# Kernel optimization log

Hardware: AMD Instinct MI355X
Metric: run time of the kernel (lower is better)

Reference implementation:

```python
import jax, jax.numpy as jnp
import numpy as np

N = 100000      # nodes
E = 1600000     # edges (no self-loops by construction)
DIN, DH, DOUT = 128, 128, 64
EPS = 1e-8      # torch cosine_similarity eps
LN_EPS = 1e-5


def _segsum(v, idx, n=N):
    return jax.ops.segment_sum(v, idx, num_segments=n)


def att_coef(feats, row, col):
    """Edge-wise cosine-sim attention + degree norm + self-loop append (torch no_grad block).
    Returns fixed-shape (row2, col2, vals2) of length E+N; filtered edges get weight 0
    (equivalent to removal for all scatter_add / message-passing math)."""
    dot = jnp.einsum('ed,ed->e', feats[row], feats[col])            # [E]
    nrm = jnp.maximum(jnp.linalg.norm(feats, axis=1), EPS)          # [N]
    sims = dot / (nrm[row] * nrm[col])
    keep = sims >= 0.1                                              # row!=col guaranteed
    sims = jnp.where(keep, sims, 0.0)
    deg = _segsum(sims, row)
    dinv = jnp.where(deg > 0, deg ** -0.5, 0.0)                     # inf -> 0
    sims = dinv[row] * sims * dinv[col]
    deg_new = _segsum(keep.astype(feats.dtype), col) + 1.0          # [N], >= 1
    self_val = 1.0 / deg_new
    vals = jnp.where(keep, jnp.exp(sims), 0.0)                      # removed edges -> 0
    sl = jnp.arange(N)
    row2 = jnp.concatenate([row, sl])
    col2 = jnp.concatenate([col, sl])
    vals2 = jnp.concatenate([vals, jnp.exp(self_val)])
    return row2, col2, vals2


def gcn_conv(x, row, col, w, W, b):
    """PyG GCNConv (normalize=True, add_self_loops=False) with given edge_weight."""
    h = x @ W                                                        # [N, out]
    deg = _segsum(w, col)
    dinv = jnp.where(deg > 0, deg ** -0.5, 0.0)
    norm = dinv[row] * w * dinv[col]                                 # [E+N]
    out = _segsum(norm[:, None] * h[row], col)                       # scatter to targets
    return out + b


def layer_norm(x, g, b):
    mu = jnp.mean(x, axis=-1, keepdims=True)
    var = jnp.mean((x - mu) ** 2, axis=-1, keepdims=True)
    return (x - mu) * jax.lax.rsqrt(var + LN_EPS) * g + b


def setup_inputs() -> dict:
    key = jax.random.key(0)
    ks = jax.random.split(key, 6)
    x = jax.random.normal(ks[0], (N, DIN), jnp.float32)
    row = jax.random.randint(ks[1], (E,), 0, N)
    col = jax.random.randint(ks[2], (E,), 0, N)
    col = jnp.where(col == row, (col + 1) % N, col)                  # no self-loops
    s1 = float(np.sqrt(6.0 / (DIN + DH)))                            # glorot
    s2 = float(np.sqrt(6.0 / (DH + DOUT)))
    W1 = jax.random.uniform(ks[3], (DIN, DH), jnp.float32, -s1, s1)
    W2 = jax.random.uniform(ks[4], (DH, DOUT), jnp.float32, -s2, s2)
    return dict(x=x, row=row, col=col,
                W1=W1, b1=jnp.zeros((DH,), jnp.float32),
                ln_g=jnp.ones((DH,), jnp.float32), ln_b=jnp.zeros((DH,), jnp.float32),
                W2=W2, b2=jnp.zeros((DOUT,), jnp.float32))


def reference(x, row, col, W1, b1, ln_g, ln_b, W2, b2):
    # layer 1: att_coef (no_grad) -> GCNConv -> LayerNorm -> ReLU (dropout is eval no-op)
    r2, c2, v2 = att_coef(jax.lax.stop_gradient(x), row, col)
    h = gcn_conv(x, r2, c2, v2, W1, b1)
    h = jax.nn.relu(layer_norm(h, ln_g, ln_b))
    # layer 2: att_coef on updated features (original edge list), final conv + log_softmax
    r2, c2, v2 = att_coef(jax.lax.stop_gradient(h), row, col)
    out = gcn_conv(h, r2, c2, v2, W2, b2)
    return jax.nn.log_softmax(out, axis=-1)
```

## Files before the change

### kernel.cpp

```cpp
#include <hip/hip_runtime.h>
#include <math.h>

#define EPSF 1e-8f
#define LN_EPS 1e-5f
#define BL_MARGIN 0.002f

#define BKT_SH 9
#define CHUNK 4096
#define DCAP 16384

typedef unsigned int  u32;
typedef unsigned short u16;
typedef _Float16 h2_t __attribute__((ext_vector_type(2)));
typedef _Float16 half8_t __attribute__((ext_vector_type(8)));
typedef float f32x4_t __attribute__((ext_vector_type(4)));

static __device__ inline u32 pack_h2(float a, float b) {
    h2_t h; h.x = (_Float16)a; h.y = (_Float16)b;
    return __builtin_bit_cast(u32, h);
}
static __device__ inline float h2lo(u32 u) {
    return (float)__builtin_bit_cast(h2_t, u).x;
}
static __device__ inline float h2hi(u32 u) {
    return (float)__builtin_bit_cast(h2_t, u).y;
}

static __device__ inline f32x4_t mfma16(uint4 a, uint4 b, f32x4_t c) {
    return __builtin_amdgcn_mfma_f32_16x16x32_f16(
        __builtin_bit_cast(half8_t, a), __builtin_bit_cast(half8_t, b), c, 0, 0, 0);
}

__global__ __launch_bounds__(256) void cast_norm_k(const float* __restrict__ feat,
    u32* __restrict__ fhf, float* __restrict__ nrm, int n) {
    int wid  = (blockIdx.x * 256 + threadIdx.x) >> 6;
    int lane = threadIdx.x & 63;
    if (wid >= n) return;
    float2 v = *(const float2*)(feat + (size_t)wid * 128 + lane * 2);
    float s = v.x * v.x + v.y * v.y;
    #pragma unroll
    for (int off = 32; off; off >>= 1) s += __shfl_xor(s, off, 64);
    float nv = fmaxf(sqrtf(s), EPSF);
    float inv = 1.0f / nv;
    fhf[(size_t)wid * 64 + lane] = pack_h2(v.x * inv, v.y * inv);
    if (lane == 0) nrm[wid] = nv;
}


__global__ __launch_bounds__(256) void hist_k(const int* __restrict__ col,
                                              int* __restrict__ bcnt, int ecnt) {
    __shared__ int lc[256];
    lc[threadIdx.x] = 0; __syncthreads();
    for (int e = blockIdx.x * 256 + threadIdx.x; e < ecnt; e += gridDim.x * 256)
        atomicAdd(&lc[col[e] >> BKT_SH], 1);
    __syncthreads();
    int v = lc[threadIdx.x];
    if (v) atomicAdd(&bcnt[threadIdx.x], v);
}

__global__ __launch_bounds__(256) void bscan_k(const int* __restrict__ bcnt,
    int* __restrict__ bstart, int* __restrict__ bcur) {
    __shared__ int tmp[256];
    int t = threadIdx.x;
    int v = bcnt[t];
    tmp[t] = v; __syncthreads();
    for (int off = 1; off < 256; off <<= 1) {
        int a = (t >= off) ? tmp[t - off] : 0;
        __syncthreads();
        tmp[t] += a;
        __syncthreads();
    }
    int ex = tmp[t] - v;
    bstart[t] = ex; bcur[t] = ex;
    if (t == 255) bstart[256] = tmp[255];
}

__global__ __launch_bounds__(256) void binfill_k(const int* __restrict__ row,
    const int* __restrict__ col, int* __restrict__ bcur,
    int2* __restrict__ ebuf, int ecnt) {
    __shared__ int lc[256], ls[256], cur[256], gbase[256];
    __shared__ int2 pairs[CHUNK];
    __shared__ int dstv[CHUNK];
    int t = threadIdx.x;
    int e0 = blockIdx.x * CHUNK;
    int m = min(CHUNK, ecnt - e0);
    lc[t] = 0; cur[t] = 0; __syncthreads();
    int myc[CHUNK / 256], myr[CHUNK / 256];
    #pragma unroll
    for (int i = 0; i < CHUNK / 256; ++i) {
        int idx = t + i * 256;
        if (idx < m) {
            myc[i] = col[e0 + idx];
            myr[i] = row[e0 + idx];
            atomicAdd(&lc[myc[i] >> BKT_SH], 1);
        }
    }
    __syncthreads();
    int v = lc[t];
    ls[t] = v; __syncthreads();
    for (int off = 1; off < 256; off <<= 1) {
        int a = (t >= off) ? ls[t - off] : 0;
        __syncthreads();
        ls[t] += a;
        __syncthreads();
    }
    int ex = ls[t] - v;
    __syncthreads();
    ls[t] = ex;
    if (v) gbase[t] = atomicAdd(&bcur[t], v);
    __syncthreads();
    #pragma unroll
    for (int i = 0; i < CHUNK / 256; ++i) {
        int idx = t + i * 256;
        if (idx < m) {
            int b = myc[i] >> BKT_SH;
            int s = ls[b] + atomicAdd(&cur[b], 1);
            pairs[s] = make_int2(myc[i], myr[i]);
            dstv[s]  = gbase[b] + (s - ls[b]);
        }
    }
    __syncthreads();
    for (int s = t; s < m; s += 256)
        ebuf[dstv[s]] = pairs[s];
}

__global__ __launch_bounds__(256) void bucket_csr_k(const int2* __restrict__ ebuf,
    const int* __restrict__ bstart, int* __restrict__ startAll,
    int* __restrict__ cntAll, int* __restrict__ rowAll, int n) {
    __shared__ int cnt[512], lst[512], cur[512];
    __shared__ int rowbuf[DCAP];
    int b = blockIdx.x, t = threadIdx.x;
    int c0 = b << BKT_SH;
    int s0 = bstart[b], s1 = bstart[b + 1];
    int m = s1 - s0;
    cnt[t] = 0; cnt[t + 256] = 0; cur[t] = 0; cur[t + 256] = 0;
    __syncthreads();
    for (int i = t; i < m; i += 256)
        atomicAdd(&cnt[ebuf[s0 + i].x - c0], 1);
    __syncthreads();
    int v0 = cnt[t], v1 = cnt[t + 256];
    lst[t] = v0; lst[t + 256] = v1; __syncthreads();
    for (int off = 1; off < 256; off <<= 1) {
        int a0 = (t >= off) ? lst[t - off] : 0;
        int a1 = (t >= off) ? lst[256 + t - off] : 0;
        __syncthreads();
        lst[t] += a0; lst[t + 256] += a1;
        __syncthreads();
    }
    int h0 = lst[255];
    int e0x = lst[t] - v0;
    int e1x = lst[t + 256] - v1 + h0;
    __syncthreads();
    lst[t] = e0x; lst[t + 256] = e1x;
    __syncthreads();
    #pragma unroll
    for (int half = 0; half < 2; ++half) {
        int i = t + half * 256;
        int c = c0 + i;
        if (c < n) { startAll[c] = s0 + lst[i]; cntAll[c] = cnt[i]; }
    }
    if (m <= DCAP) {
        for (int i = t; i < m; i += 256) {
            int2 p = ebuf[s0 + i];
            int ci = p.x - c0;
            int pos = lst[ci] + atomicAdd(&cur[ci], 1);
            rowbuf[pos] = p.y;
        }
        __syncthreads();
        for (int i = t; i < m; i += 256)
            rowAll[s0 + i] = rowbuf[i];
    } else {
        for (int i = t; i < m; i += 256) {
            int2 p = ebuf[s0 + i];
            int ci = p.x - c0;
            int pos = lst[ci] + atomicAdd(&cur[ci], 1);
            rowAll[s0 + pos] = p.y;
        }
    }
}

__global__ __launch_bounds__(256) void edge_dot_mf_k(const u32* __restrict__ fhf,
    const float* __restrict__ feat32,
    const int* __restrict__ rowAll, const int* __restrict__ startAll,
    const int* __restrict__ cntAll, const float* __restrict__ nrm,
    float* __restrict__ sims, float* __restrict__ deg1, int n) {
    int wid  = (blockIdx.x * 256 + threadIdx.x) >> 6;
    int lane = threadIdx.x & 63;
    if (wid >= n) return;
    int s0 = startAll[wid], cnt = cntAll[wid];
    if (cnt == 0) return;
    int lr = lane & 15;
    int kq = lane >> 4;
    const u32* fcp = fhf + (size_t)wid * 64 + kq * 4;
    uint4 a0 = *(const uint4*)(fcp);
    uint4 a1 = *(const uint4*)(fcp + 16);
    uint4 a2 = *(const uint4*)(fcp + 32);
    uint4 a3 = *(const uint4*)(fcp + 48);
    float nc = nrm[wid];
    int cm1 = cnt - 1;
    for (int jj = 0; jj < cnt; jj += 32) {
        int e1 = jj + lr;
        int r1 = rowAll[s0 + min(e1, cm1)];
        const u32* fr1 = fhf + (size_t)r1 * 64 + kq * 4;
        uint4 b0 = *(const uint4*)(fr1);
        uint4 b1 = *(const uint4*)(fr1 + 16);
        uint4 b2 = *(const uint4*)(fr1 + 32);
        uint4 b3 = *(const uint4*)(fr1 + 48);
        bool g2 = (jj + 16) < cnt;
        int e2 = jj + 16 + lr;
        int r2 = 0;
        uint4 c0, c1, c2, c3;
        if (g2) {
            r2 = rowAll[s0 + min(e2, cm1)];
            const u32* fr2 = fhf + (size_t)r2 * 64 + kq * 4;
            c0 = *(const uint4*)(fr2);
            c1 = *(const uint4*)(fr2 + 16);
            c2 = *(const uint4*)(fr2 + 32);
            c3 = *(const uint4*)(fr2 + 48);
        }
        f32x4_t acc = {0.f, 0.f, 0.f, 0.f};
        acc = mfma16(a0, b0, acc);
        acc = mfma16(a1, b1, acc);
        acc = mfma16(a2, b2, acc);
        acc = mfma16(a3, b3, acc);
        float p1 = acc[0];
        bool act1 = (kq == 0) && (e1 < cnt);
        float p2 = 0.0f;
        bool act2 = false;
        if (g2) {
            f32x4_t acc2 = {0.f, 0.f, 0.f, 0.f};
            acc2 = mfma16(a0, c0, acc2);
            acc2 = mfma16(a1, c1, acc2);
            acc2 = mfma16(a2, c2, acc2);
            acc2 = mfma16(a3, c3, acc2);
            p2 = acc2[0];
            act2 = (kq == 0) && (e2 < cnt);
        }
        unsigned long long bl = __ballot(act1 && fabsf(p1 - 0.1f) < BL_MARGIN);
        while (bl) {
            int src = __ffsll((unsigned long long)bl) - 1; bl &= bl - 1ull;
            int rt = __shfl(r1, src, 64);
            float2 xa = *(const float2*)(feat32 + (size_t)rt * 128 + lane * 2);
            float2 xb = *(const float2*)(feat32 + (size_t)wid * 128 + lane * 2);
            float s2 = xa.x * xb.x + xa.y * xb.y;
            #pragma unroll
            for (int off = 32; off; off >>= 1) s2 += __shfl_xor(s2, off, 64);
            float pf = s2 / (nrm[rt] * nc);
            if (lane == src) p1 = pf;
        }
        unsigned long long bl2 = __ballot(act2 && fabsf(p2 - 0.1f) < BL_MARGIN);
        while (bl2) {
            int src = __ffsll((unsigned long long)bl2) - 1; bl2 &= bl2 - 1ull;
            int rt = __shfl(r2, src, 64);
            float2 xa = *(const float2*)(feat32 + (size_t)rt * 128 + lane * 2);
            float2 xb = *(const float2*)(feat32 + (size_t)wid * 128 + lane * 2);
            float s2 = xa.x * xb.x + xa.y * xb.y;
            #pragma unroll
            for (int off = 32; off; off >>= 1) s2 += __shfl_xor(s2, off, 64);
            float pf = s2 / (nrm[rt] * nc);
            if (lane == src) p2 = pf;
        }
        if (act1) {
            float kv = (p1 >= 0.1f) ? p1 : 0.0f;
            sims[s0 + e1] = kv;
            if (kv > 0.0f) atomicAdd(&deg1[r1], kv);
        }
        if (act2) {
            float kv = (p2 >= 0.1f) ? p2 : 0.0f;
            sims[s0 + e2] = kv;
            if (kv > 0.0f) atomicAdd(&deg1[r2], kv);
        }
    }
}

__global__ __launch_bounds__(256) void edge_c_csr_k(const float* __restrict__ sims,
    const int* __restrict__ rowAll, const int* __restrict__ startAll,
    const int* __restrict__ cntAll, const float* __restrict__ deg1,
    int2* __restrict__ kv, int* __restrict__ cntK, float* __restrict__ dinv2,
    float* __restrict__ cself, int n) {
    int wid  = (blockIdx.x * 256 + threadIdx.x) >> 6;
    int lane = threadIdx.x & 63;
    if (wid >= n) return;
    int s0 = startAll[wid], cnt = cntAll[wid];
    float degc = deg1[wid];
    float d1c = (degc > 0.0f) ? 1.0f / sqrtf(degc) : 0.0f;
    float vsum = 0.0f; int kc = 0;
    for (int jj = 0; jj < cnt; jj += 64) {
        int j = jj + lane;
        bool keep = false; int r = 0; float v = 0.0f;
        if (j < cnt) {
            float s = sims[s0 + j];
            if (s > 0.0f) {
                r = rowAll[s0 + j];
                float dr = 1.0f / sqrtf(deg1[r]);
                v = expf(dr * s * d1c);
                keep = true;
            }
        }
        unsigned long long m = __ballot(keep ? 1 : 0);
        if (keep) {
            int pre = __popcll(m & ((1ull << lane) - 1ull));
            int2 pk; pk.x = r; pk.y = __float_as_int(v);
            kv[s0 + kc + pre] = pk;
            vsum += v;
        }
        kc += __popcll(m);
    }
    #pragma unroll
    for (int off = 32; off; off >>= 1) vsum += __shfl_xor(vsum, off, 64);
    if (lane == 0) {
        float ws_ = expf(1.0f / ((float)kc + 1.0f));
        float dg = ws_ + vsum;
        float di = 1.0f / sqrtf(dg);
        dinv2[wid] = di;
        cself[wid] = di * ws_;
        cntK[wid]  = kc;
    }
}


__global__ __launch_bounds__(256) void gemm128_k(const float* __restrict__ A,
    const float* __restrict__ W, const float* __restrict__ scale,
    float* __restrict__ out, int n) {
    __shared__ float Ws[128 * 64];
    int colBase = blockIdx.y * 64;
    for (int i = threadIdx.x; i < 128 * 64 / 4; i += 256) {
        int k = i >> 4, c4 = i & 15;
        ((float4*)Ws)[i] = *(const float4*)(W + k * 128 + colBase + c4 * 4);
    }
    __syncthreads();
    const int TPN = 16;
    int group = threadIdx.x / TPN;
    int tin   = threadIdx.x % TPN;
    int nid   = (blockIdx.x * 16 + group) * 4;
    if (nid >= n) return;
    int dbase = tin * 4;
    int nm1 = n - 1;
    const float4* a0 = (const float4*)(A + (size_t)min(nid,     nm1) * 128);
    const float4* a1 = (const float4*)(A + (size_t)min(nid + 1, nm1) * 128);
    const float4* a2 = (const float4*)(A + (size_t)min(nid + 2, nm1) * 128);
    const float4* a3 = (const float4*)(A + (size_t)min(nid + 3, nm1) * 128);
    float4 acc0 = {0,0,0,0}, acc1 = {0,0,0,0}, acc2 = {0,0,0,0}, acc3 = {0,0,0,0};
    #pragma unroll 2
    for (int k4 = 0; k4 < 32; ++k4) {
        const float* wr = Ws + (k4 * 4) * 64 + dbase;
        float4 w0 = *(const float4*)(wr);
        float4 w1 = *(const float4*)(wr + 64);
        float4 w2 = *(const float4*)(wr + 128);
        float4 w3 = *(const float4*)(wr + 192);
        float4 v0 = a0[k4], v1 = a1[k4], v2 = a2[k4], v3 = a3[k4];
        acc0.x += v0.x*w0.x + v0.y*w1.x + v0.z*w2.x + v0.w*w3.x;
        acc0.y += v0.x*w0.y + v0.y*w1.y + v0.z*w2.y + v0.w*w3.y;
        acc0.z += v0.x*w0.z + v0.y*w1.z + v0.z*w2.z + v0.w*w3.z;
        acc0.w += v0.x*w0.w + v0.y*w1.w + v0.z*w2.w + v0.w*w3.w;
        acc1.x += v1.x*w0.x + v1.y*w1.x + v1.z*w2.x + v1.w*w3.x;
        acc1.y += v1.x*w0.y + v1.y*w1.y + v1.z*w2.y + v1.w*w3.y;
        acc1.z += v1.x*w0.z + v1.y*w1.z + v1.z*w2.z + v1.w*w3.z;
        acc1.w += v1.x*w0.w + v1.y*w1.w + v1.z*w2.w + v1.w*w3.w;
        acc2.x += v2.x*w0.x + v2.y*w1.x + v2.z*w2.x + v2.w*w3.x;
        acc2.y += v2.x*w0.y + v2.y*w1.y + v2.z*w2.y + v2.w*w3.y;
        acc2.z += v2.x*w0.z + v2.y*w1.z + v2.z*w2.z + v2.w*w3.z;
        acc2.w += v2.x*w0.w + v2.y*w1.w + v2.z*w2.w + v2.w*w3.w;
        acc3.x += v3.x*w0.x + v3.y*w1.x + v3.z*w2.x + v3.w*w3.x;
        acc3.y += v3.x*w0.y + v3.y*w1.y + v3.z*w2.y + v3.w*w3.y;
        acc3.z += v3.x*w0.z + v3.y*w1.z + v3.z*w2.z + v3.w*w3.z;
        acc3.w += v3.x*w0.w + v3.y*w1.w + v3.z*w2.w + v3.w*w3.w;
    }
    float4 accs[4] = {acc0, acc1, acc2, acc3};
    #pragma unroll
    for (int i = 0; i < 4; ++i) {
        if (nid + i < n) {
            float sc = scale[nid + i];
            float4 r; r.x = accs[i].x * sc; r.y = accs[i].y * sc;
            r.z = accs[i].z * sc; r.w = accs[i].w * sc;
            *(float4*)(out + (size_t)(nid + i) * 128 + colBase + dbase) = r;
        }
    }
}

__global__ __launch_bounds__(256) void gemm64_hf_k(const float* __restrict__ A,
    const float* __restrict__ W, const float* __restrict__ scale,
    u32* __restrict__ outhf, int n) {
    __shared__ float Ws[128 * 32];
    int colBase = blockIdx.y * 32;
    for (int i = threadIdx.x; i < 128 * 32 / 4; i += 256) {
        int k = i >> 3, c4 = i & 7;
        ((float4*)Ws)[i] = *(const float4*)(W + k * 64 + colBase + c4 * 4);
    }
    __syncthreads();
    const int TPN = 8;
    int group = threadIdx.x / TPN;
    int tin   = threadIdx.x % TPN;
    int nid   = (blockIdx.x * 32 + group) * 4;
    if (nid >= n) return;
    int dbase = tin * 4;
    int nm1 = n - 1;
    const float4* a0 = (const float4*)(A + (size_t)min(nid,     nm1) * 128);
    const float4* a1 = (const float4*)(A + (size_t)min(nid + 1, nm1) * 128);
    const float4* a2 = (const float4*)(A + (size_t)min(nid + 2, nm1) * 128);
    const float4* a3 = (const float4*)(A + (size_t)min(nid + 3, nm1) * 128);
    float4 acc0 = {0,0,0,0}, acc1 = {0,0,0,0}, acc2 = {0,0,0,0}, acc3 = {0,0,0,0};
    #pragma unroll 2
    for (int k4 = 0; k4 < 32; ++k4) {
        const float* wr = Ws + (k4 * 4) * 32 + dbase;
        float4 w0 = *(const float4*)(wr);
        float4 w1 = *(const float4*)(wr + 32);
        float4 w2 = *(const float4*)(wr + 64);
        float4 w3 = *(const float4*)(wr + 96);
        float4 v0 = a0[k4], v1 = a1[k4], v2 = a2[k4], v3 = a3[k4];
        acc0.x += v0.x*w0.x + v0.y*w1.x + v0.z*w2.x + v0.w*w3.x;
        acc0.y += v0.x*w0.y + v0.y*w1.y + v0.z*w2.y + v0.w*w3.y;
        acc0.z += v0.x*w0.z + v0.y*w1.z + v0.z*w2.z + v0.w*w3.z;
        acc0.w += v0.x*w0.w + v0.y*w1.w + v0.z*w2.w + v0.w*w3.w;
        acc1.x += v1.x*w0.x + v1.y*w1.x + v1.z*w2.x + v1.w*w3.x;
        acc1.y += v1.x*w0.y + v1.y*w1.y + v1.z*w2.y + v1.w*w3.y;
        acc1.z += v1.x*w0.z + v1.y*w1.z + v1.z*w2.z + v1.w*w3.z;
        acc1.w += v1.x*w0.w + v1.y*w1.w + v1.z*w2.w + v1.w*w3.w;
        acc2.x += v2.x*w0.x + v2.y*w1.x + v2.z*w2.x + v2.w*w3.x;
        acc2.y += v2.x*w0.y + v2.y*w1.y + v2.z*w2.y + v2.w*w3.y;
        acc2.z += v2.x*w0.z + v2.y*w1.z + v2.z*w2.z + v2.w*w3.z;
        acc2.w += v2.x*w0.w + v2.y*w1.w + v2.z*w2.w + v2.w*w3.w;
        acc3.x += v3.x*w0.x + v3.y*w1.x + v3.z*w2.x + v3.w*w3.x;
        acc3.y += v3.x*w0.y + v3.y*w1.y + v3.z*w2.y + v3.w*w3.y;
        acc3.z += v3.x*w0.z + v3.y*w1.z + v3.z*w2.z + v3.w*w3.z;
        acc3.w += v3.x*w0.w + v3.y*w1.w + v3.z*w2.w + v3.w*w3.w;
    }
    float4 accs[4] = {acc0, acc1, acc2, acc3};
    #pragma unroll
    for (int i = 0; i < 4; ++i) {
        if (nid + i < n) {
            float sc = scale[nid + i];
            u32 o0 = pack_h2(accs[i].x * sc, accs[i].y * sc);
            u32 o1 = pack_h2(accs[i].z * sc, accs[i].w * sc);
            *(uint2*)(outhf + (size_t)(nid + i) * 32 + (colBase >> 1) + tin * 2)
                = make_uint2(o0, o1);
        }
    }
}


__global__ __launch_bounds__(256) void gather_ln_k(const float* __restrict__ hs,
    const int2* __restrict__ kv, const int* __restrict__ startAll,
    const int* __restrict__ cntK, const float* __restrict__ dinv2,
    const float* __restrict__ cself, const float* __restrict__ bias,
    const float* __restrict__ g, const float* __restrict__ bln,
    float* __restrict__ outbuf, u32* __restrict__ outhf,
    float* __restrict__ nrm, int n) {
    int wid = (blockIdx.x * 256 + threadIdx.x) >> 5;
    int l   = threadIdx.x & 31;
    if (wid >= n) return;
    int s0 = startAll[wid], k = cntK[wid];
    float4 acc = {0,0,0,0};
    int j = 0;
    for (; j + 7 < k; j += 8) {
        int2 p0 = kv[s0+j],   p1 = kv[s0+j+1], p2 = kv[s0+j+2], p3 = kv[s0+j+3];
        int2 p4 = kv[s0+j+4], p5 = kv[s0+j+5], p6 = kv[s0+j+6], p7 = kv[s0+j+7];
        float4 h0 = *(const float4*)(hs + (size_t)p0.x * 128 + l * 4);
        float4 h1 = *(const float4*)(hs + (size_t)p1.x * 128 + l * 4);
        float4 h2v = *(const float4*)(hs + (size_t)p2.x * 128 + l * 4);
        float4 h3 = *(const float4*)(hs + (size_t)p3.x * 128 + l * 4);
        float4 h4 = *(const float4*)(hs + (size_t)p4.x * 128 + l * 4);
        float4 h5 = *(const float4*)(hs + (size_t)p5.x * 128 + l * 4);
        float4 h6 = *(const float4*)(hs + (size_t)p6.x * 128 + l * 4);
        float4 h7 = *(const float4*)(hs + (size_t)p7.x * 128 + l * 4);
        float v0 = __int_as_float(p0.y), v1 = __int_as_float(p1.y);
        float v2 = __int_as_float(p2.y), v3 = __int_as_float(p3.y);
        float v4 = __int_as_float(p4.y), v5 = __int_as_float(p5.y);
        float v6 = __int_as_float(p6.y), v7 = __int_as_float(p7.y);
        acc.x += v0*h0.x + v1*h1.x + v2*h2v.x + v3*h3.x
               + v4*h4.x + v5*h5.x + v6*h6.x + v7*h7.x;
        acc.y += v0*h0.y + v1*h1.y + v2*h2v.y + v3*h3.y
               + v4*h4.y + v5*h5.y + v6*h6.y + v7*h7.y;
        acc.z += v0*h0.z + v1*h1.z + v2*h2v.z + v3*h3.z
               + v4*h4.z + v5*h5.z + v6*h6.z + v7*h7.z;
        acc.w += v0*h0.w + v1*h1.w + v2*h2v.w + v3*h3.w
               + v4*h4.w + v5*h5.w + v6*h6.w + v7*h7.w;
    }
    for (; j < k; ++j) {
        int2 p0 = kv[s0 + j];
        float4 h0 = *(const float4*)(hs + (size_t)p0.x * 128 + l * 4);
        float v0 = __int_as_float(p0.y);
        acc.x += v0*h0.x; acc.y += v0*h0.y; acc.z += v0*h0.z; acc.w += v0*h0.w;
    }
    float di = dinv2[wid], cs = cself[wid];
    float4 hsv = *(const float4*)(hs + (size_t)wid * 128 + l * 4);
    float4 vb  = *(const float4*)(bias + l * 4);
    float x0 = di*acc.x + cs*hsv.x + vb.x;
    float x1 = di*acc.y + cs*hsv.y + vb.y;
    float x2 = di*acc.z + cs*hsv.z + vb.z;
    float x3 = di*acc.w + cs*hsv.w + vb.w;
    float s = x0 + x1 + x2 + x3;
    #pragma unroll
    for (int off = 16; off; off >>= 1) s += __shfl_xor(s, off, 64);
    float mu = s * (1.0f / 128.0f);
    float d0 = x0 - mu, d1 = x1 - mu, d2 = x2 - mu, d3 = x3 - mu;
    float vv = d0*d0 + d1*d1 + d2*d2 + d3*d3;
    #pragma unroll
    for (int off = 16; off; off >>= 1) vv += __shfl_xor(vv, off, 64);
    float rstd = 1.0f / sqrtf(vv * (1.0f / 128.0f) + LN_EPS);
    float4 vg  = *(const float4*)(g + l * 4);
    float4 vbl = *(const float4*)(bln + l * 4);
    float y0 = fmaxf(d0 * rstd * vg.x + vbl.x, 0.0f);
    float y1 = fmaxf(d1 * rstd * vg.y + vbl.y, 0.0f);
    float y2 = fmaxf(d2 * rstd * vg.z + vbl.z, 0.0f);
    float y3 = fmaxf(d3 * rstd * vg.w + vbl.w, 0.0f);
    float4 yo; yo.x = y0; yo.y = y1; yo.z = y2; yo.w = y3;
    *(float4*)(outbuf + (size_t)wid * 128 + l * 4) = yo;
    float ns = y0*y0 + y1*y1 + y2*y2 + y3*y3;
    #pragma unroll
    for (int off = 16; off; off >>= 1) ns += __shfl_xor(ns, off, 64);
    float nv = fmaxf(sqrtf(ns), EPSF);
    float inv = 1.0f / nv;
    uint2 oh; oh.x = pack_h2(y0 * inv, y1 * inv); oh.y = pack_h2(y2 * inv, y3 * inv);
    *(uint2*)(outhf + (size_t)wid * 64 + l * 2) = oh;
    if (l == 0) nrm[wid] = nv;
}

__global__ __launch_bounds__(256) void gather_lsm_hf_k(const u32* __restrict__ g2s,
    const int2* __restrict__ kv, const int* __restrict__ startAll,
    const int* __restrict__ cntK, const float* __restrict__ dinv2,
    const float* __restrict__ cself, const float* __restrict__ b2,
    float* __restrict__ out, int n) {
    int wid = (blockIdx.x * 256 + threadIdx.x) >> 5;
    int l   = threadIdx.x & 31;
    if (wid >= n) return;
    int s0 = startAll[wid], k = cntK[wid];
    float acc0 = 0.f, acc1 = 0.f;
    int j = 0;
    for (; j + 7 < k; j += 8) {
        int2 p0 = kv[s0+j],   p1 = kv[s0+j+1], p2 = kv[s0+j+2], p3 = kv[s0+j+3];
        int2 p4 = kv[s0+j+4], p5 = kv[s0+j+5], p6 = kv[s0+j+6], p7 = kv[s0+j+7];
        u32 g0 = g2s[(size_t)p0.x * 32 + l];
        u32 g1 = g2s[(size_t)p1.x * 32 + l];
        u32 g2 = g2s[(size_t)p2.x * 32 + l];
        u32 g3 = g2s[(size_t)p3.x * 32 + l];
        u32 g4 = g2s[(size_t)p4.x * 32 + l];
        u32 g5 = g2s[(size_t)p5.x * 32 + l];
        u32 g6 = g2s[(size_t)p6.x * 32 + l];
        u32 g7 = g2s[(size_t)p7.x * 32 + l];
        float v0 = __int_as_float(p0.y), v1 = __int_as_float(p1.y);
        float v2 = __int_as_float(p2.y), v3 = __int_as_float(p3.y);
        float v4 = __int_as_float(p4.y), v5 = __int_as_float(p5.y);
        float v6 = __int_as_float(p6.y), v7 = __int_as_float(p7.y);
        acc0 += v0*h2lo(g0) + v1*h2lo(g1) + v2*h2lo(g2) + v3*h2lo(g3)
              + v4*h2lo(g4) + v5*h2lo(g5) + v6*h2lo(g6) + v7*h2lo(g7);
        acc1 += v0*h2hi(g0) + v1*h2hi(g1) + v2*h2hi(g2) + v3*h2hi(g3)
              + v4*h2hi(g4) + v5*h2hi(g5) + v6*h2hi(g6) + v7*h2hi(g7);
    }
    for (; j < k; ++j) {
        int2 p0 = kv[s0 + j];
        u32 g0 = g2s[(size_t)p0.x * 32 + l];
        float v0 = __int_as_float(p0.y);
        acc0 += v0 * h2lo(g0); acc1 += v0 * h2hi(g0);
    }
    float di = dinv2[wid], cs = cself[wid];
    u32 gsu = g2s[(size_t)wid * 32 + l];
    float2 vb = *(const float2*)(b2 + l * 2);
    float v0 = di * acc0 + cs * h2lo(gsu) + vb.x;
    float v1 = di * acc1 + cs * h2hi(gsu) + vb.y;
    float m = fmaxf(v0, v1);
    #pragma unroll
    for (int off = 16; off; off >>= 1) m = fmaxf(m, __shfl_xor(m, off, 64));
    float e = expf(v0 - m) + expf(v1 - m);
    #pragma unroll
    for (int off = 16; off; off >>= 1) e += __shfl_xor(e, off, 64);
    float lse = m + logf(e);
    *(float2*)(out + (size_t)wid * 64 + l * 2) = make_float2(v0 - lse, v1 - lse);
}


extern "C" void kernel_launch(void* const* d_in, const int* in_sizes, int n_in,
                              void* d_out, int out_size, void* d_ws, size_t ws_size,
                              hipStream_t stream) {
    (void)n_in; (void)out_size; (void)ws_size;
    const float* x   = (const float*)d_in[0];
    const int*   row = (const int*)d_in[1];
    const int*   col = (const int*)d_in[2];
    const float* W1  = (const float*)d_in[3];
    const float* b1  = (const float*)d_in[4];
    const float* lng = (const float*)d_in[5];
    const float* lnb = (const float*)d_in[6];
    const float* W2  = (const float*)d_in[7];
    const float* b2  = (const float*)d_in[8];
    float* out = (float*)d_out;

    const int N = in_sizes[0] / 128;
    const int E = in_sizes[1];

    int*   cntAll   = (int*)d_ws;
    int*   startAll = cntAll + N;
    int*   bcnt     = startAll + N;
    int*   bstart   = bcnt + 256;
    int*   bcur     = bstart + 257;
    float* nrm      = (float*)(bcnt + 1024);
    float* deg1     = nrm + N;
    float* dinv2    = deg1 + N;
    float* cself    = dinv2 + N;
    int*   cntK     = (int*)(cself + N);
    int*   rowAll   = cntK + N;
    int2*  kvp      = (int2*)(rowAll + E);
    u32*   fhf      = (u32*)(kvp + E);
    u32*   g2shf    = fhf + (size_t)64 * N;
    float* big      = (float*)(g2shf + (size_t)32 * N);
    float* sims     = big;
    float* hs       = big;
    float* h2       = big + (size_t)128 * N;
    int2*  ebuf     = kvp;

    const int waveBlocks  = (N + 3) / 4;
    const int halfBlocks  = (N + 7) / 8;
    const int NB          = (N + 511) >> 9;

    hipMemsetAsync(bcnt, 0, 256 * sizeof(int), stream);
    hist_k<<<256, 256, 0, stream>>>(col, bcnt, E);
    bscan_k<<<1, 256, 0, stream>>>(bcnt, bstart, bcur);
    binfill_k<<<(E + CHUNK - 1) / CHUNK, 256, 0, stream>>>(row, col, bcur, ebuf, E);
    bucket_csr_k<<<NB, 256, 0, stream>>>(ebuf, bstart, startAll, cntAll, rowAll, N);

    hipMemsetAsync(deg1, 0, (size_t)N * sizeof(float), stream);
    cast_norm_k<<<waveBlocks, 256, 0, stream>>>(x, fhf, nrm, N);
    edge_dot_mf_k<<<waveBlocks, 256, 0, stream>>>(fhf, x, rowAll, startAll, cntAll, nrm,
                                                  sims, deg1, N);
    edge_c_csr_k<<<waveBlocks, 256, 0, stream>>>(sims, rowAll, startAll, cntAll, deg1,
                                                 kvp, cntK, dinv2, cself, N);
    gemm128_k<<<dim3((N + 63) / 64, 2), 256, 0, stream>>>(x, W1, dinv2, hs, N);
    gather_ln_k<<<halfBlocks, 256, 0, stream>>>(hs, kvp, startAll, cntK, dinv2, cself,
                                                b1, lng, lnb, h2, fhf, nrm, N);

    hipMemsetAsync(deg1, 0, (size_t)N * sizeof(float), stream);
    edge_dot_mf_k<<<waveBlocks, 256, 0, stream>>>(fhf, h2, rowAll, startAll, cntAll, nrm,
                                                  sims, deg1, N);
    edge_c_csr_k<<<waveBlocks, 256, 0, stream>>>(sims, rowAll, startAll, cntAll, deg1,
                                                 kvp, cntK, dinv2, cself, N);
    gemm64_hf_k<<<dim3((N + 127) / 128, 2), 256, 0, stream>>>(h2, W2, dinv2, g2shf, N);
    gather_lsm_hf_k<<<halfBlocks, 256, 0, stream>>>(g2shf, kvp, startAll, cntK, dinv2,
                                                    cself, b2, out, N);
}
```

Baseline: 616.6 us.

## Flatten edge cosine-dot kernel to fixed 32 edges per wave

Replaces the per-node (per-column) wave mapping in the edge similarity kernel with a flat mapping where each wave handles 32 consecutive CSR edges. To support this, bucket_csr_k now also materialises a colAll array holding each edge's target. The MFMA now multiplies 16 distinct column vectors against 16 row vectors and reads the diagonal of the result. This removes load imbalance and the idle lanes that come from low-degree nodes with partial 32-edge chunks. In exchange, every wave reloads the column features instead of reusing one node's vector, and the CSR build writes an extra E-sized array.

```diff
diff --git a/kernel.cpp b/kernel.cpp
--- a/kernel.cpp
+++ b/kernel.cpp
@@ -29,6 +29,9 @@
 static __device__ inline f32x4_t mfma16(uint4 a, uint4 b, f32x4_t c) {
     return __builtin_amdgcn_mfma_f32_16x16x32_f16(
         __builtin_bit_cast(half8_t, a), __builtin_bit_cast(half8_t, b), c, 0, 0, 0);
+}
+static __device__ inline float sel4(f32x4_t a, int m) {
+    return m == 0 ? a[0] : m == 1 ? a[1] : m == 2 ? a[2] : a[3];
 }
 
 __global__ __launch_bounds__(256) void cast_norm_k(const float* __restrict__ feat,
@@ -126,7 +129,8 @@
 
 __global__ __launch_bounds__(256) void bucket_csr_k(const int2* __restrict__ ebuf,
     const int* __restrict__ bstart, int* __restrict__ startAll,
-    int* __restrict__ cntAll, int* __restrict__ rowAll, int n) {
+    int* __restrict__ cntAll, int* __restrict__ rowAll, int* __restrict__ colAll,
+    int n) {
     __shared__ int cnt[512], lst[512], cur[512];
     __shared__ int rowbuf[DCAP];
     int b = blockIdx.x, t = threadIdx.x;
@@ -169,107 +173,116 @@
         __syncthreads();
         for (int i = t; i < m; i += 256)
             rowAll[s0 + i] = rowbuf[i];
+        __syncthreads();
+        #pragma unroll
+        for (int half = 0; half < 2; ++half) {
+            int i = t + half * 256;
+            int base = lst[i], cn = cnt[i], cc = c0 + i;
+            for (int k2 = 0; k2 < cn; ++k2) rowbuf[base + k2] = cc;
+        }
+        __syncthreads();
+        for (int i = t; i < m; i += 256)
+            colAll[s0 + i] = rowbuf[i];
     } else {
         for (int i = t; i < m; i += 256) {
             int2 p = ebuf[s0 + i];
             int ci = p.x - c0;
             int pos = lst[ci] + atomicAdd(&cur[ci], 1);
             rowAll[s0 + pos] = p.y;
-        }
-    }
-}
-
-__global__ __launch_bounds__(256) void edge_dot_mf_k(const u32* __restrict__ fhf,
-    const float* __restrict__ feat32,
-    const int* __restrict__ rowAll, const int* __restrict__ startAll,
-    const int* __restrict__ cntAll, const float* __restrict__ nrm,
-    float* __restrict__ sims, float* __restrict__ deg1, int n) {
-    int wid  = (blockIdx.x * 256 + threadIdx.x) >> 6;
+            colAll[s0 + pos] = p.x;
+        }
+    }
+}
+
+__global__ __launch_bounds__(256) void edge_dot_flat_k(const u32* __restrict__ fhf,
+    const float* __restrict__ feat32, const int* __restrict__ rowAll,
+    const int* __restrict__ colAll, const float* __restrict__ nrm,
+    float* __restrict__ sims, float* __restrict__ deg1, int ecnt) {
+    int wv   = (blockIdx.x * 256 + threadIdx.x) >> 6;
     int lane = threadIdx.x & 63;
-    if (wid >= n) return;
-    int s0 = startAll[wid], cnt = cntAll[wid];
-    if (cnt == 0) return;
-    int lr = lane & 15;
-    int kq = lane >> 4;
-    const u32* fcp = fhf + (size_t)wid * 64 + kq * 4;
-    uint4 a0 = *(const uint4*)(fcp);
-    uint4 a1 = *(const uint4*)(fcp + 16);
-    uint4 a2 = *(const uint4*)(fcp + 32);
-    uint4 a3 = *(const uint4*)(fcp + 48);
-    float nc = nrm[wid];
-    int cm1 = cnt - 1;
-    for (int jj = 0; jj < cnt; jj += 32) {
-        int e1 = jj + lr;
-        int r1 = rowAll[s0 + min(e1, cm1)];
-        const u32* fr1 = fhf + (size_t)r1 * 64 + kq * 4;
-        uint4 b0 = *(const uint4*)(fr1);
-        uint4 b1 = *(const uint4*)(fr1 + 16);
-        uint4 b2 = *(const uint4*)(fr1 + 32);
-        uint4 b3 = *(const uint4*)(fr1 + 48);
-        bool g2 = (jj + 16) < cnt;
-        int e2 = jj + 16 + lr;
-        int r2 = 0;
-        uint4 c0, c1, c2, c3;
-        if (g2) {
-            r2 = rowAll[s0 + min(e2, cm1)];
-            const u32* fr2 = fhf + (size_t)r2 * 64 + kq * 4;
-            c0 = *(const uint4*)(fr2);
-            c1 = *(const uint4*)(fr2 + 16);
-            c2 = *(const uint4*)(fr2 + 32);
-            c3 = *(const uint4*)(fr2 + 48);
-        }
-        f32x4_t acc = {0.f, 0.f, 0.f, 0.f};
-        acc = mfma16(a0, b0, acc);
-        acc = mfma16(a1, b1, acc);
-        acc = mfma16(a2, b2, acc);
-        acc = mfma16(a3, b3, acc);
-        float p1 = acc[0];
-        bool act1 = (kq == 0) && (e1 < cnt);
-        float p2 = 0.0f;
-        bool act2 = false;
-        if (g2) {
-            f32x4_t acc2 = {0.f, 0.f, 0.f, 0.f};
-            acc2 = mfma16(a0, c0, acc2);
-            acc2 = mfma16(a1, c1, acc2);
-            acc2 = mfma16(a2, c2, acc2);
-            acc2 = mfma16(a3, c3, acc2);
-            p2 = acc2[0];
-            act2 = (kq == 0) && (e2 < cnt);
-        }
-        unsigned long long bl = __ballot(act1 && fabsf(p1 - 0.1f) < BL_MARGIN);
-        while (bl) {
-            int src = __ffsll((unsigned long long)bl) - 1; bl &= bl - 1ull;
-            int rt = __shfl(r1, src, 64);
-            float2 xa = *(const float2*)(feat32 + (size_t)rt * 128 + lane * 2);
-            float2 xb = *(const float2*)(feat32 + (size_t)wid * 128 + lane * 2);
-            float s2 = xa.x * xb.x + xa.y * xb.y;
-            #pragma unroll
-            for (int off = 32; off; off >>= 1) s2 += __shfl_xor(s2, off, 64);
-            float pf = s2 / (nrm[rt] * nc);
-            if (lane == src) p1 = pf;
-        }
-        unsigned long long bl2 = __ballot(act2 && fabsf(p2 - 0.1f) < BL_MARGIN);
-        while (bl2) {
-            int src = __ffsll((unsigned long long)bl2) - 1; bl2 &= bl2 - 1ull;
-            int rt = __shfl(r2, src, 64);
-            float2 xa = *(const float2*)(feat32 + (size_t)rt * 128 + lane * 2);
-            float2 xb = *(const float2*)(feat32 + (size_t)wid * 128 + lane * 2);
-            float s2 = xa.x * xb.x + xa.y * xb.y;
-            #pragma unroll
-            for (int off = 32; off; off >>= 1) s2 += __shfl_xor(s2, off, 64);
-            float pf = s2 / (nrm[rt] * nc);
-            if (lane == src) p2 = pf;
-        }
-        if (act1) {
-            float kv = (p1 >= 0.1f) ? p1 : 0.0f;
-            sims[s0 + e1] = kv;
-            if (kv > 0.0f) atomicAdd(&deg1[r1], kv);
-        }
-        if (act2) {
-            float kv = (p2 >= 0.1f) ? p2 : 0.0f;
-            sims[s0 + e2] = kv;
-            if (kv > 0.0f) atomicAdd(&deg1[r2], kv);
-        }
+    int e0 = wv * 32;
+    if (e0 >= ecnt) return;
+    int lr = lane & 15, kq = lane >> 4;
+    bool diag = (kq == (lr >> 2));
+    int m3 = lane & 3;
+    int em1 = ecnt - 1;
+
+    int e1 = e0 + lr, e2 = e0 + 16 + lr;
+    int e1c = min(e1, em1), e2c = min(e2, em1);
+    int r1 = rowAll[e1c], c1 = colAll[e1c];
+    int r2 = rowAll[e2c], c2 = colAll[e2c];
+    const u32* pa1 = fhf + (size_t)c1 * 64 + kq * 4;
+    const u32* pb1 = fhf + (size_t)r1 * 64 + kq * 4;
+    const u32* pa2 = fhf + (size_t)c2 * 64 + kq * 4;
+    const u32* pb2 = fhf + (size_t)r2 * 64 + kq * 4;
+    uint4 a10 = *(const uint4*)(pa1);
+    uint4 a11 = *(const uint4*)(pa1 + 16);
+    uint4 a12 = *(const uint4*)(pa1 + 32);
+    uint4 a13 = *(const uint4*)(pa1 + 48);
+    uint4 b10 = *(const uint4*)(pb1);
+    uint4 b11 = *(const uint4*)(pb1 + 16);
+    uint4 b12 = *(const uint4*)(pb1 + 32);
+    uint4 b13 = *(const uint4*)(pb1 + 48);
+    uint4 a20 = *(const uint4*)(pa2);
+    uint4 a21 = *(const uint4*)(pa2 + 16);
+    uint4 a22 = *(const uint4*)(pa2 + 32);
+    uint4 a23 = *(const uint4*)(pa2 + 48);
+    uint4 b20 = *(const uint4*)(pb2);
+    uint4 b21 = *(const uint4*)(pb2 + 16);
+    uint4 b22 = *(const uint4*)(pb2 + 32);
+    uint4 b23 = *(const uint4*)(pb2 + 48);
+
+    f32x4_t acc1 = {0.f, 0.f, 0.f, 0.f};
+    acc1 = mfma16(a10, b10, acc1);
+    acc1 = mfma16(a11, b11, acc1);
+    acc1 = mfma16(a12, b12, acc1);
+    acc1 = mfma16(a13, b13, acc1);
+    f32x4_t acc2 = {0.f, 0.f, 0.f, 0.f};
+    acc2 = mfma16(a20, b20, acc2);
+    acc2 = mfma16(a21, b21, acc2);
+    acc2 = mfma16(a22, b22, acc2);
+    acc2 = mfma16(a23, b23, acc2);
+
+    float p1 = sel4(acc1, m3);
+    float p2 = sel4(acc2, m3);
+    bool act1 = diag && (e1 < ecnt);
+    bool act2 = diag && (e2 < ecnt);
+
+    unsigned long long bl = __ballot(act1 && fabsf(p1 - 0.1f) < BL_MARGIN);
+    while (bl) {
+        int src = __ffsll((unsigned long long)bl) - 1; bl &= bl - 1ull;
+        int rt = __shfl(r1, src, 64);
+        int ct = __shfl(c1, src, 64);
+        float2 xa = *(const float2*)(feat32 + (size_t)rt * 128 + lane * 2);
+        float2 xb = *(const float2*)(feat32 + (size_t)ct * 128 + lane * 2);
+        float s2 = xa.x * xb.x + xa.y * xb.y;
+        #pragma unroll
+        for (int off = 32; off; off >>= 1) s2 += __shfl_xor(s2, off, 64);
+        float pf = s2 / (nrm[rt] * nrm[ct]);
+        if (lane == src) p1 = pf;
+    }
+    unsigned long long bl2 = __ballot(act2 && fabsf(p2 - 0.1f) < BL_MARGIN);
+    while (bl2) {
+        int src = __ffsll((unsigned long long)bl2) - 1; bl2 &= bl2 - 1ull;
+        int rt = __shfl(r2, src, 64);
+        int ct = __shfl(c2, src, 64);
+        float2 xa = *(const float2*)(feat32 + (size_t)rt * 128 + lane * 2);
+        float2 xb = *(const float2*)(feat32 + (size_t)ct * 128 + lane * 2);
+        float s2 = xa.x * xb.x + xa.y * xb.y;
+        #pragma unroll
+        for (int off = 32; off; off >>= 1) s2 += __shfl_xor(s2, off, 64);
+        float pf = s2 / (nrm[rt] * nrm[ct]);
+        if (lane == src) p2 = pf;
+    }
+    if (act1) {
+        float kv = (p1 >= 0.1f) ? p1 : 0.0f;
+        sims[e1] = kv;
+        if (kv > 0.0f) atomicAdd(&deg1[r1], kv);
+    }
+    if (act2) {
+        float kv = (p2 >= 0.1f) ? p2 : 0.0f;
+        sims[e2] = kv;
+        if (kv > 0.0f) atomicAdd(&deg1[r2], kv);
     }
 }
 
@@ -598,7 +611,8 @@
     float* cself    = dinv2 + N;
     int*   cntK     = (int*)(cself + N);
     int*   rowAll   = cntK + N;
-    int2*  kvp      = (int2*)(rowAll + E);
+    int*   colAll   = rowAll + E;
+    int2*  kvp      = (int2*)(colAll + E);
     u32*   fhf      = (u32*)(kvp + E);
     u32*   g2shf    = fhf + (size_t)64 * N;
     float* big      = (float*)(g2shf + (size_t)32 * N);
@@ -609,18 +623,20 @@
 
     const int waveBlocks  = (N + 3) / 4;
     const int halfBlocks  = (N + 7) / 8;
+    const int flatBlocks  = (E + 127) / 128;
     const int NB          = (N + 511) >> 9;
 
     hipMemsetAsync(bcnt, 0, 256 * sizeof(int), stream);
     hist_k<<<256, 256, 0, stream>>>(col, bcnt, E);
     bscan_k<<<1, 256, 0, stream>>>(bcnt, bstart, bcur);
     binfill_k<<<(E + CHUNK - 1) / CHUNK, 256, 0, stream>>>(row, col, bcur, ebuf, E);
-    bucket_csr_k<<<NB, 256, 0, stream>>>(ebuf, bstart, startAll, cntAll, rowAll, N);
+    bucket_csr_k<<<NB, 256, 0, stream>>>(ebuf, bstart, startAll, cntAll, rowAll,
+                                         colAll, N);
 
     hipMemsetAsync(deg1, 0, (size_t)N * sizeof(float), stream);
     cast_norm_k<<<waveBlocks, 256, 0, stream>>>(x, fhf, nrm, N);
-    edge_dot_mf_k<<<waveBlocks, 256, 0, stream>>>(fhf, x, rowAll, startAll, cntAll, nrm,
-                                                  sims, deg1, N);
+    edge_dot_flat_k<<<flatBlocks, 256, 0, stream>>>(fhf, x, rowAll, colAll, nrm,
+                                                    sims, deg1, E);
     edge_c_csr_k<<<waveBlocks, 256, 0, stream>>>(sims, rowAll, startAll, cntAll, deg1,
                                                  kvp, cntK, dinv2, cself, N);
     gemm128_k<<<dim3((N + 63) / 64, 2), 256, 0, stream>>>(x, W1, dinv2, hs, N);
@@ -628,8 +644,8 @@
                                                 b1, lng, lnb, h2, fhf, nrm, N);
 
     hipMemsetAsync(deg1, 0, (size_t)N * sizeof(float), stream);
-    edge_dot_mf_k<<<waveBlocks, 256, 0, stream>>>(fhf, h2, rowAll, startAll, cntAll, nrm,
-                                                  sims, deg1, N);
+    edge_dot_flat_k<<<flatBlocks, 256, 0, stream>>>(fhf, h2, rowAll, colAll, nrm,
+                                                    sims, deg1, E);
     edge_c_csr_k<<<waveBlocks, 256, 0, stream>>>(sims, rowAll, startAll, cntAll, deg1,
                                                  kvp, cntK, dinv2, cself, N);
     gemm64_hf_k<<<dim3((N + 127) / 128, 2), 256, 0, stream>>>(h2, W2, dinv2, g2shf, N);
```

Result: no change. 608.7 us (-1.3%).
